# Optimization experiments

Hardware: AMD Instinct MI355X
Metric: run time of the kernel (lower is better)

## Reference

```python
import jax, jax.numpy as jnp
import numpy as np

NEG_SLOPE = 0.2  # PyG GATConv default


def _gat_layer(x, src, dst, W, a_src, a_dst, b, heads, concat):
    # x: [N, F_in], W: [F_in, H*C], a_src/a_dst: [H, C], b: [H*C] or [C]
    N = x.shape[0]
    h = (x @ W).reshape(N, heads, -1)                      # [N, H, C]
    s_n = jnp.sum(h * a_src, axis=-1)                      # [N, H] per-node src score
    d_n = jnp.sum(h * a_dst, axis=-1)                      # [N, H] per-node dst score
    e = jax.nn.leaky_relu(s_n[src] + d_n[dst], NEG_SLOPE)  # [E, H] edge logits
    # segment softmax over incoming edges of each destination node
    m = jax.ops.segment_max(e, dst, num_segments=N)        # [N, H]
    ex = jnp.exp(e - m[dst])                               # [E, H]
    denom = jax.ops.segment_sum(ex, dst, num_segments=N)   # [N, H]
    alpha = ex / denom[dst]                                # [E, H]
    out = jax.ops.segment_sum(h[src] * alpha[:, :, None], dst, num_segments=N)  # [N, H, C]
    if concat:
        out = out.reshape(N, -1)
    else:
        out = out.mean(axis=1)
    return out + b


def setup_inputs() -> dict:
    key = jax.random.key(0)
    ks = jax.random.split(key, 12)
    N, E = 50000, 800000
    F_in, Ch, H, F_out = 128, 32, 4, 64
    x = jax.random.normal(ks[0], (N, F_in), dtype=jnp.float32)
    edge_index = jax.random.randint(ks[1], (2, E), 0, N, dtype=jnp.int64)
    # layer 1 params (glorot-ish scale)
    W1 = jax.random.normal(ks[2], (F_in, H * Ch), dtype=jnp.float32) * (1.0 / np.sqrt(F_in))
    a1_src = jax.random.normal(ks[3], (H, Ch), dtype=jnp.float32) * (1.0 / np.sqrt(Ch))
    a1_dst = jax.random.normal(ks[4], (H, Ch), dtype=jnp.float32) * (1.0 / np.sqrt(Ch))
    b1 = jnp.zeros((H * Ch,), dtype=jnp.float32)
    # layer 2 params (heads=1)
    W2 = jax.random.normal(ks[5], (H * Ch, F_out), dtype=jnp.float32) * (1.0 / np.sqrt(H * Ch))
    a2_src = jax.random.normal(ks[6], (1, F_out), dtype=jnp.float32) * (1.0 / np.sqrt(F_out))
    a2_dst = jax.random.normal(ks[7], (1, F_out), dtype=jnp.float32) * (1.0 / np.sqrt(F_out))
    b2 = jnp.zeros((F_out,), dtype=jnp.float32)
    return {"x": x, "edge_index": edge_index, "drpt": 0,
            "W1": W1, "a1_src": a1_src, "a1_dst": a1_dst, "b1": b1,
            "W2": W2, "a2_src": a2_src, "a2_dst": a2_dst, "b2": b2}


def reference(x, edge_index, drpt, W1, a1_src, a1_dst, b1, W2, a2_src, a2_dst, b2):
    N = x.shape[0]
    # PyG GATConv adds self-loops by default
    loops = jnp.arange(N, dtype=edge_index.dtype)
    src = jnp.concatenate([edge_index[0], loops])
    dst = jnp.concatenate([edge_index[1], loops])
    h = _gat_layer(x, src, dst, W1, a1_src, a1_dst, b1, heads=4, concat=True)
    h = jax.nn.relu(h)
    # F.dropout with training=False (eval) is identity; drpt unused at inference
    out = _gat_layer(h, src, dst, W2, a2_src, a2_dst, b2, heads=1, concat=True)
    return out
```

## Files before the change

### kernel.cpp

```cpp
#include <hip/hip_runtime.h>
#include <hip/hip_fp16.h>


typedef _Float16 half8 __attribute__((ext_vector_type(8)));
typedef float f32x4 __attribute__((ext_vector_type(4)));

constexpr int BCAP = 8192;
constexpr int NTHB = 256;
constexpr int NBIN = 256;
constexpr unsigned SENT = 0xFFFFFFFFu;

__device__ __forceinline__ int wave_iscan(int v, int lane) {
    #pragma unroll
    for (int off = 1; off < 64; off <<= 1) {
        int t = __shfl_up(v, off);
        if (lane >= off) v += t;
    }
    return v;
}

__global__ __launch_bounds__(256) void prep_wt(const float* __restrict__ W1,
                                               const float* __restrict__ W2,
                                               _Float16* __restrict__ Wt1,
                                               _Float16* __restrict__ Wt2,
                                               int* __restrict__ gcur) {
    int i = blockIdx.x * blockDim.x + threadIdx.x;
    if (i < 128 * 128) {
        int c = i >> 7, k = i & 127;
        Wt1[i] = (_Float16)W1[k * 128 + c];
    } else if (i < 128 * 128 + 64 * 128) {
        int j = i - 128 * 128;
        int c = j >> 7, k = j & 127;
        Wt2[j] = (_Float16)W2[k * 64 + c];
    } else if (i < 128 * 128 + 64 * 128 + 512) {
        gcur[i - (128 * 128 + 64 * 128)] = 0;
    }
}

__global__ __launch_bounds__(256) void fused_bin_gemm1(
        const int* __restrict__ ei, int* __restrict__ gcur,
        int* __restrict__ gtot, unsigned int* __restrict__ packed,
        int E, int nb, int Epb,
        const float* __restrict__ X, const _Float16* __restrict__ Wt,
        const float* __restrict__ a_src, const float* __restrict__ a_dst,
        _Float16* __restrict__ Yh, float* __restrict__ s,
        float* __restrict__ d, int N) {
    __shared__ __align__(16) char smem[17408];
    const int tid  = threadIdx.x;
    const int lane = tid & 63;
    const int wv   = tid >> 6;

    if (blockIdx.x < NBIN) {
        int* hist = (int*)smem;
        int* scn  = hist + 256;
        int* cur  = scn + 256;
        int* gbs  = cur + 256;
        int* wsum = gbs + 256;
        unsigned int* staged = (unsigned int*)(wsum + 16);
        const int blk = blockIdx.x;
        const int e0  = blk * Epb;
        int ecnt = E - e0; ecnt = ecnt < 0 ? 0 : (ecnt > Epb ? Epb : ecnt);

        hist[tid] = 0;
        __syncthreads();
        for (int k = tid; k < ecnt; k += 256)
            atomicAdd(&hist[ei[E + e0 + k] >> 8], 1);
        __syncthreads();

        int v   = hist[tid];
        int isc = wave_iscan(v, lane);
        if (lane == 63) wsum[wv] = isc;
        __syncthreads();
        int add = 0;
        #pragma unroll
        for (int i = 0; i < 4; ++i) add += (i < wv) ? wsum[i] : 0;
        isc += add;
        scn[tid] = isc;
        if (tid < nb && v) {
            int pad = (v + 15) & ~15;
            int b0  = atomicAdd(&gcur[tid], pad);
            if (b0 > BCAP - pad) b0 = BCAP - pad;
            gbs[tid] = b0;
            atomicAdd(&gtot[tid], v);
        }
        cur[tid] = isc - v;
        __syncthreads();

        for (int k = tid; k < ecnt; k += 256) {
            int src = ei[e0 + k], dst = ei[E + e0 + k];
            int pos = atomicAdd(&cur[dst >> 8], 1);
            staged[pos] = ((unsigned)(dst & 255) << 16) | (unsigned)src;
        }
        __syncthreads();

        const int sg = lane >> 4;
        const int sl = lane & 15;
        for (int base = 0; base < nb; base += 16) {
            int b = base + wv * 4 + sg;
            if (b < nb) {
                int len = hist[b];
                if (len) {
                    int rs  = scn[b] - len;
                    int pad = (len + 15) & ~15;
                    unsigned int* dp = &packed[(size_t)b * BCAP + gbs[b]];
                    for (int k = sl; k < pad; k += 16)
                        dp[k] = (k < len) ? staged[rs + k] : SENT;
                }
            }
        }
        return;
    }

    constexpr int NT = 8, FOUT = 128;
    auto xs = (_Float16(*)[136])smem;
    const int row0 = (blockIdx.x - NBIN) * 64;

    for (int c = tid; c < 2048; c += 256) {
        int r = c >> 5, c4 = c & 31;
        float4 v = make_float4(0.f, 0.f, 0.f, 0.f);
        if (row0 + r < N)
            v = reinterpret_cast<const float4*>(X)[(size_t)(row0 + r) * 32 + c4];
        _Float16* p = &xs[r][c4 * 4];
        p[0] = (_Float16)v.x; p[1] = (_Float16)v.y;
        p[2] = (_Float16)v.z; p[3] = (_Float16)v.w;
    }
    __syncthreads();

    const int l15 = lane & 15;
    const int lg  = lane >> 4;

    f32x4 acc[NT];
    #pragma unroll
    for (int n = 0; n < NT; ++n) acc[n] = (f32x4){0.f, 0.f, 0.f, 0.f};

    const half8* WtV = reinterpret_cast<const half8*>(Wt);
    #pragma unroll
    for (int ks = 0; ks < 4; ++ks) {
        half8 a = *reinterpret_cast<const half8*>(&xs[wv * 16 + l15][ks * 32 + lg * 8]);
        #pragma unroll
        for (int n = 0; n < NT; ++n) {
            half8 b = WtV[(size_t)(n * 16 + l15) * 16 + ks * 4 + lg];
            acc[n] = __builtin_amdgcn_mfma_f32_16x16x32_f16(a, b, acc[n], 0, 0, 0);
        }
    }

    #pragma unroll
    for (int n = 0; n < NT; ++n)
        #pragma unroll
        for (int r = 0; r < 4; ++r)
            xs[wv * 16 + lg * 4 + r][n * 16 + l15] = (_Float16)acc[n][r];

    #pragma unroll
    for (int p = 0; p < 4; ++p) {
        int idx = p * 64 + lane;
        int row = idx >> 4, c4 = idx & 15;
        int grow = row0 + wv * 16 + row;
        uint4 vv = *reinterpret_cast<const uint4*>(&xs[wv * 16 + row][c4 * 8]);
        if (grow < N)
            *reinterpret_cast<uint4*>(&Yh[(size_t)grow * FOUT + c4 * 8]) = vv;
    }

    {
        int row = lane >> 2, head = lane & 3;
        int grow = row0 + wv * 16 + row;
        float ls = 0.f, ld = 0.f;
        #pragma unroll
        for (int q = 0; q < 4; ++q) {
            half8 hv = *reinterpret_cast<const half8*>(&xs[wv * 16 + row][head * 32 + q * 8]);
            #pragma unroll
            for (int j = 0; j < 8; ++j) {
                float h = (float)hv[j];
                ls = fmaf(h, a_src[head * 32 + q * 8 + j], ls);
                ld = fmaf(h, a_dst[head * 32 + q * 8 + j], ld);
            }
        }
        if (grow < N) {
            s[(size_t)grow * 4 + head] = ls;
            d[(size_t)grow * 4 + head] = ld;
        }
    }
}

__global__ __launch_bounds__(256) void build_csr(const unsigned int* __restrict__ packed,
                                                 const int* __restrict__ gcur,
                                                 const int* __restrict__ gtot,
                                                 unsigned short* __restrict__ csr,
                                                 int* __restrict__ row_end,
                                                 int N, int nb) {
    __shared__ int deg[256];
    __shared__ int scn[256];
    __shared__ int wsum[4];
    __shared__ unsigned short lcsr[BCAP + 256];
    const int b    = blockIdx.x;
    const int tid  = threadIdx.x;
    const int lane = tid & 63;
    const int wv   = tid >> 6;
    const int node = (b << 8) + tid;
    const bool real = node < N;

    int nodes_t = N - tid * NTHB;
    nodes_t = nodes_t < 0 ? 0 : (nodes_t > NTHB ? NTHB : nodes_t);
    int vall = (tid < nb) ? gtot[tid] + nodes_t : 0;
    int isc  = wave_iscan(vall, lane);
    if (lane == 63) wsum[wv] = isc;
    __syncthreads();
    int add = 0;
    #pragma unroll
    for (int i = 0; i < 4; ++i) add += (i < wv) ? wsum[i] : 0;
    scn[tid] = isc + add;
    deg[tid] = real ? 1 : 0;
    __syncthreads();

    int nodes_b = N - b * NTHB;
    nodes_b = nodes_b < 0 ? 0 : (nodes_b > NTHB ? NTHB : nodes_b);
    const int gb = scn[b] - gtot[b] - nodes_b;
    int ext = gcur[b]; if (ext > BCAP) ext = BCAP;

    const unsigned int* pk = &packed[(size_t)b * BCAP];
    for (int k = tid; k < ext; k += 256) {
        unsigned int p = pk[k];
        if (p != SENT) atomicAdd(&deg[p >> 16], 1);
    }
    __syncthreads();

    int v = deg[tid];
    isc = wave_iscan(v, lane);
    if (lane == 63) wsum[wv] = isc;
    __syncthreads();
    add = 0;
    #pragma unroll
    for (int i = 0; i < 4; ++i) add += (i < wv) ? wsum[i] : 0;
    const int incl  = isc + add;
    const int start = incl - v;
    const int tot   = wsum[0] + wsum[1] + wsum[2] + wsum[3];

    if (real) {
        lcsr[start] = (unsigned short)node;
        row_end[node] = gb + incl;
    }
    deg[tid] = start + (real ? 1 : 0);
    __syncthreads();

    for (int k = tid; k < ext; k += 256) {
        unsigned int p = pk[k];
        if (p == SENT) continue;
        int pos = atomicAdd(&deg[p >> 16], 1);
        lcsr[pos] = (unsigned short)(p & 0xffffu);
    }
    __syncthreads();

    for (int k = tid; k < tot; k += 256)
        csr[gb + k] = lcsr[k];
}

__device__ __forceinline__ float edge_w(float x) {
    return __expf(x > 0.f ? x : 0.2f * x);
}

__device__ __forceinline__ void acc8(float* acc, uint4 r, float w) {
    const __half2* h2 = reinterpret_cast<const __half2*>(&r);
    #pragma unroll
    for (int j = 0; j < 4; ++j) {
        float2 f = __half22float2(h2[j]);
        acc[2 * j]     = fmaf(w, f.x, acc[2 * j]);
        acc[2 * j + 1] = fmaf(w, f.y, acc[2 * j + 1]);
    }
}

__global__ __launch_bounds__(256) void gather1_gemm2(
        const unsigned short* __restrict__ csr, const int* __restrict__ row_end,
        const float* __restrict__ s, const float* __restrict__ d,
        const _Float16* __restrict__ hh, const float* __restrict__ b1,
        const _Float16* __restrict__ Wt2,
        const float* __restrict__ a2s, const float* __restrict__ a2d,
        _Float16* __restrict__ Yh2, float* __restrict__ s2,
        float* __restrict__ d2, int N) {
    constexpr int H = 4, C = 32, CT = 128;
    __shared__ _Float16 xs[16][136];
    __shared__ float sp[16], dp[16];
    const int tid   = threadIdx.x;
    const int lane  = tid & 15;
    const int nloc  = tid >> 4;
    const int node0 = blockIdx.x * 16;
    const int node  = node0 + nloc;

    float o[8] = {0.f, 0.f, 0.f, 0.f, 0.f, 0.f, 0.f, 0.f};
    if (node < N) {
        int start = node ? row_end[node - 1] : 0;
        int end   = row_end[node];
        int c0 = lane * 8;
        int head = c0 / C;
        float dn = d[(size_t)node * H + head];
        float acc[8] = {0.f, 0.f, 0.f, 0.f, 0.f, 0.f, 0.f, 0.f};
        float den = 0.f;

        for (int k = start; k < end; k += 8) {
            int idx[8];
            float sv[8];
            uint4 rr[8];
            #pragma unroll
            for (int j = 0; j < 8; ++j) {
                int kk = k + j;
                int kc = kk < end ? kk : end - 1;
                idx[j] = csr[kc];
                sv[j]  = s[(size_t)idx[j] * H + head];
            }
            #pragma unroll
            for (int j = 0; j < 8; ++j)
                rr[j] = *reinterpret_cast<const uint4*>(&hh[(size_t)idx[j] * CT + c0]);
            #pragma unroll
            for (int j = 0; j < 8; ++j) {
                float w = edge_w(sv[j] + dn);
                if (k + j >= end) w = 0.f;
                den += w;
                acc8(acc, rr[j], w);
            }
        }
        float inv = 1.f / den;
        #pragma unroll
        for (int j = 0; j < 8; ++j)
            o[j] = fmaxf(acc[j] * inv + b1[lane * 8 + j], 0.f);
    }
    {
        union { _Float16 h[8]; uint4 u; } pk;
        #pragma unroll
        for (int j = 0; j < 8; ++j) pk.h[j] = (_Float16)o[j];
        *reinterpret_cast<uint4*>(&xs[nloc][lane * 8]) = pk.u;
    }
    if (tid < 16) { sp[tid] = 0.f; dp[tid] = 0.f; }
    __syncthreads();

    const int wv  = tid >> 6;
    const int l   = tid & 63;
    const int l15 = l & 15;
    const int lg  = l >> 4;

    f32x4 acc2 = (f32x4){0.f, 0.f, 0.f, 0.f};
    const half8* WtV = reinterpret_cast<const half8*>(Wt2);
    #pragma unroll
    for (int ks = 0; ks < 4; ++ks) {
        half8 a = *reinterpret_cast<const half8*>(&xs[l15][ks * 32 + lg * 8]);
        half8 b = WtV[(size_t)(wv * 16 + l15) * 16 + ks * 4 + lg];
        acc2 = __builtin_amdgcn_mfma_f32_16x16x32_f16(a, b, acc2, 0, 0, 0);
    }

    const int col = wv * 16 + l15;
    const float av = a2s[col], bv = a2d[col];
    #pragma unroll
    for (int r = 0; r < 4; ++r) {
        int row = lg * 4 + r;
        int gn  = node0 + row;
        if (gn < N)
            Yh2[(size_t)gn * 64 + col] = (_Float16)acc2[r];
        float lsr = acc2[r] * av, ldr = acc2[r] * bv;
        #pragma unroll
        for (int m = 1; m < 16; m <<= 1) {
            lsr += __shfl_xor(lsr, m);
            ldr += __shfl_xor(ldr, m);
        }
        if (l15 == 0) {
            atomicAdd(&sp[row], lsr);
            atomicAdd(&dp[row], ldr);
        }
    }
    __syncthreads();
    if (tid < 16 && node0 + tid < N) {
        s2[node0 + tid] = sp[tid];
        d2[node0 + tid] = dp[tid];
    }
}

template<int H, int C, bool RELU, bool OUTH>
__global__ __launch_bounds__(256) void gat_gather(const unsigned short* __restrict__ csr,
                                                  const int* __restrict__ row_end,
                                                  const float* __restrict__ s,
                                                  const float* __restrict__ d,
                                                  const _Float16* __restrict__ hh,
                                                  const float* __restrict__ b,
                                                  void* __restrict__ outp, int N) {
    constexpr int CT = H * C;
    constexpr int G  = CT / 8;
    int t = blockIdx.x * blockDim.x + threadIdx.x;
    int node = t / G;
    int lane = t % G;
    if (node >= N) return;

    int start = node ? row_end[node - 1] : 0;
    int end   = row_end[node];

    int c0 = lane * 8;
    int head = c0 / C;
    float dn = d[(size_t)node * H + head];

    float acc[8] = {0.f, 0.f, 0.f, 0.f, 0.f, 0.f, 0.f, 0.f};
    float den = 0.f;

    for (int k = start; k < end; k += 8) {
        int idx[8];
        float sv[8];
        uint4 rr[8];
        #pragma unroll
        for (int j = 0; j < 8; ++j) {
            int kk = k + j;
            int kc = kk < end ? kk : end - 1;
            idx[j] = csr[kc];
            sv[j]  = s[(size_t)idx[j] * H + head];
        }
        #pragma unroll
        for (int j = 0; j < 8; ++j)
            rr[j] = *reinterpret_cast<const uint4*>(&hh[(size_t)idx[j] * CT + c0]);
        #pragma unroll
        for (int j = 0; j < 8; ++j) {
            float w = edge_w(sv[j] + dn);
            if (k + j >= end) w = 0.f;
            den += w;
            acc8(acc, rr[j], w);
        }
    }

    float inv = 1.f / den;
    float o[8];
    #pragma unroll
    for (int j = 0; j < 8; ++j) {
        o[j] = acc[j] * inv + b[c0 + j];
        if (RELU) o[j] = fmaxf(o[j], 0.f);
    }
    if constexpr (OUTH) {
        union { _Float16 h[8]; uint4 u; } pk;
        #pragma unroll
        for (int j = 0; j < 8; ++j) pk.h[j] = (_Float16)o[j];
        _Float16* out = (_Float16*)outp;
        *reinterpret_cast<uint4*>(&out[(size_t)node * CT + c0]) = pk.u;
    } else {
        float* out = (float*)outp;
        float4* op = reinterpret_cast<float4*>(&out[(size_t)node * CT + c0]);
        op[0] = make_float4(o[0], o[1], o[2], o[3]);
        op[1] = make_float4(o[4], o[5], o[6], o[7]);
    }
}

extern "C" void kernel_launch(void* const* d_in, const int* in_sizes, int n_in,
                              void* d_out, int out_size, void* d_ws, size_t ws_size,
                              hipStream_t stream) {
    const float* x      = (const float*)d_in[0];
    const int*   ei     = (const int*)d_in[1];
    const float* W1     = (const float*)d_in[3];
    const float* a1_src = (const float*)d_in[4];
    const float* a1_dst = (const float*)d_in[5];
    const float* b1     = (const float*)d_in[6];
    const float* W2     = (const float*)d_in[7];
    const float* a2_src = (const float*)d_in[8];
    const float* a2_dst = (const float*)d_in[9];
    const float* b2     = (const float*)d_in[10];

    const int N = in_sizes[0] / 128;
    const int E = in_sizes[1] / 2;
    const int NB = (N + NTHB - 1) / NTHB;
    const int Epb = (E + NBIN - 1) / NBIN;
    const int NG1 = (N + 63) / 64;
    float* out = (float*)d_out;

    float* f = (float*)d_ws;
    _Float16* h1h = (_Float16*)f;
    _Float16* h2h = (_Float16*)(f + (size_t)N * 64);
    unsigned int* packed = (unsigned int*)h2h;
    float* s1 = f + (size_t)N * 128;
    float* d1 = f + (size_t)N * 132;
    int*   row_end = (int*)(f + (size_t)N * 136);
    int*   gcur    = row_end + N;
    int*   gtot    = gcur + 256;
    _Float16* Wt1  = (_Float16*)(gtot + 256);
    _Float16* Wt2  = Wt1 + 128 * 128;
    unsigned short* csr = (unsigned short*)(Wt2 + 64 * 128);
    float* s2 = (float*)(csr + ((E + N + 1) & ~1));
    float* d2 = s2 + N;

    prep_wt<<<98, 256, 0, stream>>>(W1, W2, Wt1, Wt2, gcur);
    fused_bin_gemm1<<<NBIN + NG1, 256, 0, stream>>>(
        ei, gcur, gtot, packed, E, NB, Epb,
        x, Wt1, a1_src, a1_dst, h1h, s1, d1, N);
    build_csr<<<NB, 256, 0, stream>>>(packed, gcur, gtot, csr, row_end, N, NB);
    gather1_gemm2<<<(N + 15) / 16, 256, 0, stream>>>(
        csr, row_end, s1, d1, h1h, b1, Wt2, a2_src, a2_dst, h2h, s2, d2, N);
    gat_gather<1, 64, false, false><<<(int)(((size_t)N * 8 + 255) / 256), 256, 0, stream>>>(
        csr, row_end, s2, d2, h2h, b2, out, N);
}
```

Measured before the change: 109.9 us.

## Drop padded sentinel binning and double binning blocks for edge partitioning

Binning blocks now reserve exactly the number of edges they hold in each destination bucket, with no 16-entry padding and no sentinel fill. The separate total counter goes away and gcur doubles as the exact per-bucket count, so build_csr no longer tests each entry for a sentinel. The number of binning blocks rises from 256 to 512, which halves the edges each block handles and adds more blocks and more atomics on gcur. With smaller per-block chunks the unaligned, unpadded writes may coalesce less well.

Result: slower. 112.4 us (+2.3%).

```diff
diff --git a/kernel.cpp b/kernel.cpp
--- a/kernel.cpp
+++ b/kernel.cpp
@@ -7,8 +7,7 @@
 
 constexpr int BCAP = 8192;
 constexpr int NTHB = 256;
-constexpr int NBIN = 256;
-constexpr unsigned SENT = 0xFFFFFFFFu;
+constexpr int NBIN = 512;
 
 __device__ __forceinline__ int wave_iscan(int v, int lane) {
     #pragma unroll
@@ -32,14 +31,14 @@
         int j = i - 128 * 128;
         int c = j >> 7, k = j & 127;
         Wt2[j] = (_Float16)W2[k * 64 + c];
-    } else if (i < 128 * 128 + 64 * 128 + 512) {
+    } else if (i < 128 * 128 + 64 * 128 + 256) {
         gcur[i - (128 * 128 + 64 * 128)] = 0;
     }
 }
 
 __global__ __launch_bounds__(256) void fused_bin_gemm1(
         const int* __restrict__ ei, int* __restrict__ gcur,
-        int* __restrict__ gtot, unsigned int* __restrict__ packed,
+        unsigned int* __restrict__ packed,
         int E, int nb, int Epb,
         const float* __restrict__ X, const _Float16* __restrict__ Wt,
         const float* __restrict__ a_src, const float* __restrict__ a_dst,
@@ -76,13 +75,8 @@
         for (int i = 0; i < 4; ++i) add += (i < wv) ? wsum[i] : 0;
         isc += add;
         scn[tid] = isc;
-        if (tid < nb && v) {
-            int pad = (v + 15) & ~15;
-            int b0  = atomicAdd(&gcur[tid], pad);
-            if (b0 > BCAP - pad) b0 = BCAP - pad;
-            gbs[tid] = b0;
-            atomicAdd(&gtot[tid], v);
-        }
+        if (tid < nb && v)
+            gbs[tid] = atomicAdd(&gcur[tid], v);
         cur[tid] = isc - v;
         __syncthreads();
 
@@ -100,11 +94,10 @@
             if (b < nb) {
                 int len = hist[b];
                 if (len) {
-                    int rs  = scn[b] - len;
-                    int pad = (len + 15) & ~15;
+                    int rs = scn[b] - len;
                     unsigned int* dp = &packed[(size_t)b * BCAP + gbs[b]];
-                    for (int k = sl; k < pad; k += 16)
-                        dp[k] = (k < len) ? staged[rs + k] : SENT;
+                    for (int k = sl; k < len; k += 16)
+                        dp[k] = staged[rs + k];
                 }
             }
         }
@@ -183,7 +176,6 @@
 
 __global__ __launch_bounds__(256) void build_csr(const unsigned int* __restrict__ packed,
                                                  const int* __restrict__ gcur,
-                                                 const int* __restrict__ gtot,
                                                  unsigned short* __restrict__ csr,
                                                  int* __restrict__ row_end,
                                                  int N, int nb) {
@@ -200,7 +192,7 @@
 
     int nodes_t = N - tid * NTHB;
     nodes_t = nodes_t < 0 ? 0 : (nodes_t > NTHB ? NTHB : nodes_t);
-    int vall = (tid < nb) ? gtot[tid] + nodes_t : 0;
+    int vall = (tid < nb) ? gcur[tid] + nodes_t : 0;
     int isc  = wave_iscan(vall, lane);
     if (lane == 63) wsum[wv] = isc;
     __syncthreads();
@@ -213,14 +205,12 @@
 
     int nodes_b = N - b * NTHB;
     nodes_b = nodes_b < 0 ? 0 : (nodes_b > NTHB ? NTHB : nodes_b);
-    const int gb = scn[b] - gtot[b] - nodes_b;
+    const int gb = scn[b] - gcur[b] - nodes_b;
     int ext = gcur[b]; if (ext > BCAP) ext = BCAP;
 
     const unsigned int* pk = &packed[(size_t)b * BCAP];
-    for (int k = tid; k < ext; k += 256) {
-        unsigned int p = pk[k];
-        if (p != SENT) atomicAdd(&deg[p >> 16], 1);
-    }
+    for (int k = tid; k < ext; k += 256)
+        atomicAdd(&deg[pk[k] >> 16], 1);
     __syncthreads();
 
     int v = deg[tid];
@@ -243,7 +233,6 @@
 
     for (int k = tid; k < ext; k += 256) {
         unsigned int p = pk[k];
-        if (p == SENT) continue;
         int pos = atomicAdd(&deg[p >> 16], 1);
         lcsr[pos] = (unsigned short)(p & 0xffffu);
     }
@@ -468,8 +457,7 @@
     float* d1 = f + (size_t)N * 132;
     int*   row_end = (int*)(f + (size_t)N * 136);
     int*   gcur    = row_end + N;
-    int*   gtot    = gcur + 256;
-    _Float16* Wt1  = (_Float16*)(gtot + 256);
+    _Float16* Wt1  = (_Float16*)(gcur + 256);
     _Float16* Wt2  = Wt1 + 128 * 128;
     unsigned short* csr = (unsigned short*)(Wt2 + 64 * 128);
     float* s2 = (float*)(csr + ((E + N + 1) & ~1));
@@ -477,9 +465,9 @@
 
     prep_wt<<<98, 256, 0, stream>>>(W1, W2, Wt1, Wt2, gcur);
     fused_bin_gemm1<<<NBIN + NG1, 256, 0, stream>>>(
-        ei, gcur, gtot, packed, E, NB, Epb,
+        ei, gcur, packed, E, NB, Epb,
         x, Wt1, a1_src, a1_dst, h1h, s1, d1, N);
-    build_csr<<<NB, 256, 0, stream>>>(packed, gcur, gtot, csr, row_end, N, NB);
+    build_csr<<<NB, 256, 0, stream>>>(packed, gcur, csr, row_end, N, NB);
     gather1_gemm2<<<(N + 15) / 16, 256, 0, stream>>>(
         csr, row_end, s1, d1, h1h, b1, Wt2, a2_src, a2_dst, h2h, s2, d2, N);
     gat_gather<1, 64, false, false><<<(int)(((size_t)N * 8 + 255) / 256), 256, 0, stream>>>(
```
